# Kernel tuning notes

Hardware: AMD Instinct MI355X
Metric: run time of the kernel (lower is better)

The kernel has to match this reference:

```python
import jax, jax.numpy as jnp
import numpy as np


def _grid_sample_bilinear_zeros(img, grid):
    """PyTorch grid_sample(mode='bilinear', padding_mode='zeros', align_corners=True).
    img: (N, C, H, W); grid: (N, Ho, Wo, 2) with last dim = (x_norm, y_norm) in [-1, 1].
    """
    N, C, H, W = img.shape
    gx = (grid[..., 0] + 1.0) * 0.5 * (W - 1)  # (N, Ho, Wo) pixel coords
    gy = (grid[..., 1] + 1.0) * 0.5 * (H - 1)
    x0 = jnp.floor(gx)
    y0 = jnp.floor(gy)
    x1 = x0 + 1.0
    y1 = y0 + 1.0
    wx1 = gx - x0
    wx0 = 1.0 - wx1
    wy1 = gy - y0
    wy0 = 1.0 - wy1

    def corner(xi, yi, wgt):
        valid = ((xi >= 0) & (xi <= W - 1) & (yi >= 0) & (yi <= H - 1)).astype(img.dtype)
        xc = jnp.clip(xi, 0, W - 1).astype(jnp.int32)
        yc = jnp.clip(yi, 0, H - 1).astype(jnp.int32)
        # per-sample fancy gather: (C,H,W)[ :, (Ho,Wo), (Ho,Wo)] -> (C,Ho,Wo)
        v = jax.vmap(lambda im, yy, xx: im[:, yy, xx])(img, yc, xc)  # (N,C,Ho,Wo)
        return v * (valid * wgt)[:, None]

    return (corner(x0, y0, wx0 * wy0) + corner(x1, y0, wx1 * wy0)
            + corner(x0, y1, wx0 * wy1) + corner(x1, y1, wx1 * wy1))


def _backwarp(x, flow):
    """x, flow: (N, C/2, H, W); flow in pixels (hor, ver). align_corners=True grid."""
    N, _, H, W = flow.shape
    hor = jnp.linspace(-1.0, 1.0, W, dtype=flow.dtype)
    ver = jnp.linspace(-1.0, 1.0, H, dtype=flow.dtype)
    base = jnp.stack([jnp.broadcast_to(hor[None, :], (H, W)),
                      jnp.broadcast_to(ver[:, None], (H, W))], axis=0)[None]  # (1,2,H,W)
    # pixel flow -> normalized flow (H != W branch of original)
    norm = jnp.array([2.0 / (W - 1.0), 2.0 / (H - 1.0)], dtype=flow.dtype).reshape(1, 2, 1, 1)
    g = (base + flow * norm).transpose(0, 2, 3, 1)  # (N,H,W,2)
    return _grid_sample_bilinear_zeros(x, g)


def setup_inputs() -> dict:
    key = jax.random.key(0)
    k1, k2 = jax.random.split(key)
    B, C, T, H, W = 2, 3, 5, 720, 1280
    x = jax.random.normal(k1, (B, C, T, H, W), dtype=jnp.float32)
    f = jax.random.normal(k2, (B, 3, T, H, W), dtype=jnp.float32)
    return {"x": x, "f": f}


def reference(x, f):
    # scale = 1, num_seq = T (interpolate branch skipped since scale == 1)
    B, C, T, H, W = x.shape
    xf = x.transpose(0, 2, 1, 3, 4).reshape(B * T, C, H, W)      # (b t) c h w
    ff = f.transpose(0, 2, 1, 3, 4).reshape(B * T, 3, H, W)
    weight = jax.nn.sigmoid(ff[:, 2:3])                           # (BT,1,H,W)
    flow = ff[:, :2]                                              # (BT,2,H,W)
    xw = _backwarp(xf, flow)                                      # warped image
    ow = _backwarp(jnp.ones_like(xf), flow) * weight              # warped ones mask
    xw = xw * weight
    def back(a):  # (b t) c h w -> b c t h w
        return a.reshape(B, T, a.shape[1], H, W).transpose(0, 2, 1, 3, 4)
    return (back(ow), back(xw))
```

## Files before the change

### kernel.cpp

```cpp
#include <hip/hip_runtime.h>

constexpr int B  = 2, C = 3, T = 5, H = 720, W = 1280;
constexpr int HW = H * W;
constexpr int CH_STRIDE = T * HW;
constexpr int OUT_HALF  = B * C * T * HW;

constexpr int TILE_W = 16;
constexpr int TILE_H = 16;
constexpr int TPW = (W / 2) / TILE_W;
constexpr int TPC = H / TILE_H;
constexpr int TPP = TPW * TPC;
constexpr int NBLK  = B * T * TPP;
constexpr int NXCD  = 8;
constexpr int CHUNK = NBLK / NXCD;

typedef float2 __attribute__((aligned(4))) f2u;

__global__ __launch_bounds__(256, 4)
void bwarp_kernel(const float* __restrict__ x, const float* __restrict__ f,
                  float* __restrict__ out)
{
    int bid = blockIdx.x;
    int swz = (bid & (NXCD - 1)) * CHUNK + (bid >> 3);

    int btu = __builtin_amdgcn_readfirstlane(swz / TPP);
    int rem = swz - btu * TPP;
    int ty  = __builtin_amdgcn_readfirstlane(rem / TPW);
    int tx  = rem - ty * TPW;
    int b   = btu / T, t = btu - b * T;
    int plane = (b * 3 * T + t) * HW;

    int lx = (int)threadIdx.x & (TILE_W - 1);
    int ly = (int)threadIdx.x >> 4;
    int xpx = (tx * TILE_W + lx) * 2;
    int h   = ty * TILE_H + ly;
    int base0 = plane + h * W + xpx;

    float2 fx2 = *(const float2*)(f + base0);
    float2 fy2 = *(const float2*)(f + base0 + CH_STRIDE);
    float2 fw2 = *(const float2*)(f + base0 + 2 * CH_STRIDE);

    int   a0[2], a1[2];
    float wA[2], wB[2], wC[2], wD[2], sig[2], o0[2];

    #pragma unroll
    for (int j = 0; j < 2; ++j) {
        float fx = j ? fx2.y : fx2.x;
        float fy = j ? fy2.y : fy2.x;
        float fw = j ? fw2.y : fw2.x;

        float gx = (float)(xpx + j) + fx;
        float gy = (float)h + fy;

        float x0f = floorf(gx), y0f = floorf(gy);
        float wx1 = gx - x0f, wx0 = 1.0f - wx1;
        float wy1 = gy - y0f, wy0 = 1.0f - wy1;
        int x0 = (int)x0f, y0 = (int)y0f;
        int x1 = x0 + 1,   y1 = y0 + 1;

        float vx0 = (x0 >= 0 && x0 < W) ? 1.0f : 0.0f;
        float vx1 = (x1 >= 0 && x1 < W) ? 1.0f : 0.0f;
        float vy0 = (y0 >= 0 && y0 < H) ? 1.0f : 0.0f;
        float vy1 = (y1 >= 0 && y1 < H) ? 1.0f : 0.0f;

        float w00 = wx0 * wy0 * vx0 * vy0;
        float w10 = wx1 * wy0 * vx1 * vy0;
        float w01 = wx0 * wy1 * vx0 * vy1;
        float w11 = wx1 * wy1 * vx1 * vy1;

        float s = 1.0f / (1.0f + __expf(-fw));
        sig[j] = s;
        o0[j]  = (w00 + w10 + w01 + w11) * s;

        bool edge = (x0 < 0) | (x0 >= W - 1);
        wA[j] = edge ? w10 : w00;
        wB[j] = edge ? w00 : w10;
        wC[j] = edge ? w11 : w01;
        wD[j] = edge ? w01 : w11;

        int xl  = min(max(x0, 0), W - 2);
        int y0c = min(max(y0, 0), H - 1);
        int y1c = min(max(y1, 0), H - 1);
        a0[j] = y0c * W + xl;
        a1[j] = y1c * W + xl;
    }

    f2u p0[3][2], p1[3][2];
    #pragma unroll
    for (int c = 0; c < 3; ++c) {
        const float* xp = x + plane + c * CH_STRIDE;
        #pragma unroll
        for (int j = 0; j < 2; ++j) {
            p0[c][j] = *(const f2u*)(xp + a0[j]);
            p1[c][j] = *(const f2u*)(xp + a1[j]);
        }
    }

    float2 ow2 = make_float2(o0[0], o0[1]);
    #pragma unroll
    for (int c = 0; c < 3; ++c) {
        float r[2];
        #pragma unroll
        for (int j = 0; j < 2; ++j) {
            float v = wA[j] * p0[c][j].x;
            v = fmaf(wB[j], p0[c][j].y, v);
            v = fmaf(wC[j], p1[c][j].x, v);
            v = fmaf(wD[j], p1[c][j].y, v);
            r[j] = v * sig[j];
        }
        *(float2*)(out + base0 + c * CH_STRIDE) = ow2;
        *(float2*)(out + OUT_HALF + base0 + c * CH_STRIDE)
            = make_float2(r[0], r[1]);
    }
}

extern "C" void kernel_launch(void* const* d_in, const int* in_sizes, int n_in,
                              void* d_out, int out_size, void* d_ws, size_t ws_size,
                              hipStream_t stream) {
    const float* x = (const float*)d_in[0];
    const float* f = (const float*)d_in[1];
    float* out = (float*)d_out;
    bwarp_kernel<<<NBLK, 256, 0, stream>>>(x, f, out);
}
```

Baseline: 380.8 us.

## Stage haloed source tile in LDS via async global_load_lds for bilinear gathers

Each block asynchronously copies a 48x28 haloed region of all three image channels into shared memory with global_load_lds, then performs the bilinear corner reads from LDS. Samples whose footprint falls outside the staged region fall back to the original global gathers. The aim is to replace scattered uncoalesced global gathers with coalesced bulk loads plus cheap LDS reads. In exchange it adds a block barrier, about 16KB of LDS per block, drops the occupancy hint, and performs some redundant halo traffic. A leftover w11 expression is dead code.

```diff
diff --git a/kernel.cpp b/kernel.cpp
--- a/kernel.cpp
+++ b/kernel.cpp
@@ -1,4 +1,6 @@
 #include <hip/hip_runtime.h>
+
+typedef unsigned int u32;
 
 constexpr int B  = 2, C = 3, T = 5, H = 720, W = 1280;
 constexpr int HW = H * W;
@@ -14,12 +16,19 @@
 constexpr int NXCD  = 8;
 constexpr int CHUNK = NBLK / NXCD;
 
+constexpr int REG_W = 48;
+constexpr int REG_H = 28;
+constexpr int REG_CH = REG_W * REG_H;
+constexpr int NF4 = 3 * REG_CH / 4;
+
 typedef float2 __attribute__((aligned(4))) f2u;
 
-__global__ __launch_bounds__(256, 4)
+__global__ __launch_bounds__(256)
 void bwarp_kernel(const float* __restrict__ x, const float* __restrict__ f,
                   float* __restrict__ out)
 {
+    __shared__ float smem[3 * REG_CH];
+
     int bid = blockIdx.x;
     int swz = (bid & (NXCD - 1)) * CHUNK + (bid >> 3);
 
@@ -29,6 +38,29 @@
     int tx  = rem - ty * TPW;
     int b   = btu / T, t = btu - b * T;
     int plane = (b * 3 * T + t) * HW;
+
+    int xs = min(max(tx * TILE_W * 2 - 8, 0), W - REG_W);
+    int ys = min(max(ty * TILE_H - 6, 0), H - REG_H);
+
+    {
+        int tid = (int)threadIdx.x;
+        const float* src = x + plane;
+        #pragma unroll
+        for (int k = 0; k < 4; ++k) {
+            int idx = tid + k * 256;
+            if (idx < NF4) {
+                int c   = idx / (REG_CH / 4);
+                int rm  = idx - c * (REG_CH / 4);
+                int ry  = rm / (REG_W / 4);
+                int rx4 = rm - ry * (REG_W / 4);
+                const float* gp = src + c * CH_STRIDE + (ys + ry) * W + xs + rx4 * 4;
+                float* lp = smem + idx * 4;
+                __builtin_amdgcn_global_load_lds(
+                    (const __attribute__((address_space(1))) u32*)gp,
+                    (__attribute__((address_space(3))) u32*)lp, 16, 0, 0);
+            }
+        }
+    }
 
     int lx = (int)threadIdx.x & (TILE_W - 1);
     int ly = (int)threadIdx.x >> 4;
@@ -40,7 +72,8 @@
     float2 fy2 = *(const float2*)(f + base0 + CH_STRIDE);
     float2 fw2 = *(const float2*)(f + base0 + 2 * CH_STRIDE);
 
-    int   a0[2], a1[2];
+    int   a0[2], a1[2], l0[2], l1[2];
+    bool  inr[2];
     float wA[2], wB[2], wC[2], wD[2], sig[2], o0[2];
 
     #pragma unroll
@@ -66,7 +99,8 @@
         float w00 = wx0 * wy0 * vx0 * vy0;
         float w10 = wx1 * wy0 * vx1 * vy0;
         float w01 = wx0 * wy1 * vx0 * vy1;
-        float w11 = wx1 * wy1 * vx1 * vy1;
+        float w11 = wx1 * wy1 * vx0 * vy1 * 0.0f + wx1 * wy1 * vx1 * vy1;
+        w11 = wx1 * wy1 * vx1 * vy1;
 
         float s = 1.0f / (1.0f + __expf(-fw));
         sig[j] = s;
@@ -83,16 +117,46 @@
         int y1c = min(max(y1, 0), H - 1);
         a0[j] = y0c * W + xl;
         a1[j] = y1c * W + xl;
+
+        int rx  = xl - xs;
+        int ry0 = y0c - ys;
+        int ry1 = y1c - ys;
+        inr[j] = ((u32)rx <= (u32)(REG_W - 2)) &
+                 ((u32)ry0 <= (u32)(REG_H - 1)) &
+                 ((u32)ry1 <= (u32)(REG_H - 1));
+        int rxc = min(max(rx, 0), REG_W - 2);
+        int r0c = min(max(ry0, 0), REG_H - 1);
+        int r1c = min(max(ry1, 0), REG_H - 1);
+        l0[j] = r0c * REG_W + rxc;
+        l1[j] = r1c * REG_W + rxc;
     }
 
-    f2u p0[3][2], p1[3][2];
+    __syncthreads();
+
+    float v00[3][2], v10[3][2], v01[3][2], v11[3][2];
     #pragma unroll
     for (int c = 0; c < 3; ++c) {
-        const float* xp = x + plane + c * CH_STRIDE;
+        const float* sm = smem + c * REG_CH;
         #pragma unroll
         for (int j = 0; j < 2; ++j) {
-            p0[c][j] = *(const f2u*)(xp + a0[j]);
-            p1[c][j] = *(const f2u*)(xp + a1[j]);
+            v00[c][j] = sm[l0[j]];
+            v10[c][j] = sm[l0[j] + 1];
+            v01[c][j] = sm[l1[j]];
+            v11[c][j] = sm[l1[j] + 1];
+        }
+    }
+
+    #pragma unroll
+    for (int j = 0; j < 2; ++j) {
+        if (!inr[j]) {
+            #pragma unroll
+            for (int c = 0; c < 3; ++c) {
+                const float* xp = x + plane + c * CH_STRIDE;
+                f2u p0 = *(const f2u*)(xp + a0[j]);
+                f2u p1 = *(const f2u*)(xp + a1[j]);
+                v00[c][j] = p0.x; v10[c][j] = p0.y;
+                v01[c][j] = p1.x; v11[c][j] = p1.y;
+            }
         }
     }
 
@@ -102,10 +166,10 @@
         float r[2];
         #pragma unroll
         for (int j = 0; j < 2; ++j) {
-            float v = wA[j] * p0[c][j].x;
-            v = fmaf(wB[j], p0[c][j].y, v);
-            v = fmaf(wC[j], p1[c][j].x, v);
-            v = fmaf(wD[j], p1[c][j].y, v);
+            float v = wA[j] * v00[c][j];
+            v = fmaf(wB[j], v10[c][j], v);
+            v = fmaf(wC[j], v01[c][j], v);
+            v = fmaf(wD[j], v11[c][j], v);
             r[j] = v * sig[j];
         }
         *(float2*)(out + base0 + c * CH_STRIDE) = ow2;
```

New measurement: 379.3 us. Within noise of the previous version (-0.4%).
